# Performance work log

Hardware: AMD Instinct MI355X
Metric: run time of the kernel (lower is better)

Reference implementation:

```python
import jax, jax.numpy as jnp
import numpy as np

EXPR_MASK_RATIO = 0.4
POS_MASK_RATIO = 0.33
MIN_VISIBLE_GENES = 10


def setup_inputs() -> dict:
    key = jax.random.key(0)
    k1, k2 = jax.random.split(key)
    expression = jax.random.normal(k1, (16, 1024, 2000), dtype=jnp.float32)
    position = jax.random.normal(k2, (16, 1024, 3), dtype=jnp.float32)
    return {"expression": expression, "position": position}


def _expression_mask(expression, key):
    # strategy == 'random': rand matrix, kthvalue threshold, mask = rand >= threshold
    B, N, G = expression.shape
    num_masked = max(1, int(G * EXPR_MASK_RATIO))
    num_masked = min(num_masked, G - MIN_VISIBLE_GENES)
    rand = jax.random.uniform(key, (B, N, G), dtype=jnp.float32)
    # torch.kthvalue(rand, G - num_masked): (G - num_masked)-th smallest value,
    # i.e. index G - num_masked - 1 of the ascending sort (keepdim=True).
    kth = jnp.sort(rand, axis=-1)[..., G - num_masked - 1 : G - num_masked]  # (B,N,1)
    return rand >= kth  # bool (B,N,G); includes the threshold element, as in torch code


def _position_mask(position, key):
    # Vectorized form of the per-(b,n) loop:
    #   r < ratio*0.3      -> mask 2 of 3 dims (randperm(3)[:2] == complement of one uniform dim)
    #   ratio*0.3 <= r < ratio -> mask 1 uniform dim
    B, N, _ = position.shape
    kr, k1, k2 = jax.random.split(key, 3)
    r = jax.random.uniform(kr, (B, N), dtype=jnp.float32)
    two = r < POS_MASK_RATIO * 0.3
    one = (r < POS_MASK_RATIO) & (~two)
    dim1 = jax.random.randint(k1, (B, N), 0, 3)  # dim masked in the 1-dim branch
    excl = jax.random.randint(k2, (B, N), 0, 3)  # dim kept in the 2-dim branch
    eye = jnp.eye(3, dtype=bool)
    m1 = eye[dim1]        # (B,N,3) one-hot
    m2 = ~eye[excl]       # (B,N,3) two hot
    false3 = jnp.zeros((B, N, 3), dtype=bool)
    return jnp.where(two[..., None], m2, jnp.where(one[..., None], m1, false3))


def reference(expression, position):
    key = jax.random.key(42)
    ke, kp = jax.random.split(key)
    expr_mask = _expression_mask(expression, ke)   # (B,N,G) bool
    pos_mask = _position_mask(position, kp)        # (B,N,3) bool
    return expr_mask, pos_mask
```

## Files before the change

kernel.cpp:

```cpp
#include <hip/hip_runtime.h>
#include <stdint.h>

#define TF_ROUND(x0, x1, r)                    \
  {                                            \
    x0 += x1;                                  \
    x1 = (x1 << (r)) | (x1 >> (32 - (r)));     \
    x1 ^= x0;                                  \
  }

__host__ __device__ inline void threefry2x32(uint32_t k0, uint32_t k1,
                                             uint32_t x0, uint32_t x1,
                                             uint32_t& o0, uint32_t& o1) {
  const uint32_t ks2 = k0 ^ k1 ^ 0x1BD11BDAu;
  x0 += k0; x1 += k1;
  TF_ROUND(x0, x1, 13) TF_ROUND(x0, x1, 15) TF_ROUND(x0, x1, 26) TF_ROUND(x0, x1, 6)
  x0 += k1; x1 += ks2 + 1u;
  TF_ROUND(x0, x1, 17) TF_ROUND(x0, x1, 29) TF_ROUND(x0, x1, 16) TF_ROUND(x0, x1, 24)
  x0 += ks2; x1 += k0 + 2u;
  TF_ROUND(x0, x1, 13) TF_ROUND(x0, x1, 15) TF_ROUND(x0, x1, 26) TF_ROUND(x0, x1, 6)
  x0 += k0; x1 += k1 + 3u;
  TF_ROUND(x0, x1, 17) TF_ROUND(x0, x1, 29) TF_ROUND(x0, x1, 16) TF_ROUND(x0, x1, 24)
  x0 += k1; x1 += ks2 + 4u;
  TF_ROUND(x0, x1, 13) TF_ROUND(x0, x1, 15) TF_ROUND(x0, x1, 26) TF_ROUND(x0, x1, 6)
  x0 += ks2; x1 += k0 + 5u;
  o0 = x0; o1 = x1;
}

__device__ inline uint32_t random_bits32(uint32_t k0, uint32_t k1, uint32_t i) {
  uint32_t y0, y1;
  threefry2x32(k0, k1, 0u, i, y0, y1);
  return y0 ^ y1;
}

constexpr int B = 16;
constexpr int N = 1024;
constexpr int G = 2000;
constexpr int NUM_ROWS = B * N;
constexpr int RANK = G - 800 - 1;
constexpr long long EXPR_ELEMS = (long long)NUM_ROWS * G;

__global__ __launch_bounds__(256) void expr_mask_kernel(int32_t* __restrict__ out,
                                                        uint32_t ke0,
                                                        uint32_t ke1) {
  __shared__ uint32_t sm[G];
  __shared__ uint32_t hist[256];
  __shared__ uint32_t scan[256];
  __shared__ uint32_t cand[256];
  __shared__ uint32_t s_cnt;
  __shared__ uint32_t s_bucket;
  __shared__ uint32_t s_kk;
  __shared__ uint32_t s_thr;

  const int row = blockIdx.x;
  const int t = threadIdx.x;
  const long long rowbase = (long long)row * G;

  hist[t] = 0u;
  if (t == 0) s_cnt = 0u;
  __syncthreads();

  for (int g = t; g < G; g += 256) {
    uint32_t bits = random_bits32(ke0, ke1, (uint32_t)(rowbase + g));
    uint32_t m = bits >> 9;
    sm[g] = m;
    atomicAdd(&hist[m >> 15], 1u);
  }
  __syncthreads();

  uint32_t v = hist[t];
  scan[t] = v;
  __syncthreads();
  for (int off = 1; off < 256; off <<= 1) {
    uint32_t add = (t >= off) ? scan[t - off] : 0u;
    __syncthreads();
    scan[t] += add;
    __syncthreads();
  }
  uint32_t incl = scan[t];
  uint32_t excl = incl - v;
  if (excl <= (uint32_t)RANK && (uint32_t)RANK < incl) {
    s_bucket = (uint32_t)t;
    s_kk = (uint32_t)RANK - excl;
  }
  __syncthreads();

  const uint32_t bucket = s_bucket;
  for (int g = t; g < G; g += 256) {
    uint32_t m = sm[g];
    if ((m >> 15) == bucket) {
      uint32_t p = atomicAdd(&s_cnt, 1u);
      if (p < 256u) cand[p] = m;
    }
  }
  __syncthreads();

  const uint32_t c = (s_cnt < 256u) ? s_cnt : 256u;
  const uint32_t kk = s_kk;
  if ((uint32_t)t < c) {
    uint32_t mv = cand[t];
    uint32_t r = 0;
    for (uint32_t j = 0; j < c; ++j) {
      uint32_t mj = cand[j];
      r += (mj < mv) || (mj == mv && j < (uint32_t)t);
    }
    if (r == kk) s_thr = mv;
  }
  __syncthreads();

  const uint32_t thr = s_thr;
  for (int g = t; g < G; g += 256) {
    out[rowbase + g] = (sm[g] >= thr) ? 1 : 0;
  }
}

__global__ __launch_bounds__(256) void pos_mask_kernel(
    int32_t* __restrict__ out,
    uint32_t kr0, uint32_t kr1,
    uint32_t ah0, uint32_t ah1, uint32_t al0, uint32_t al1,
    uint32_t bh0, uint32_t bh1, uint32_t bl0, uint32_t bl1) {
  const int i = blockIdx.x * 256 + threadIdx.x;
  if (i >= NUM_ROWS) return;

  uint32_t rb = random_bits32(kr0, kr1, (uint32_t)i);
  union { uint32_t u; float f; } cvt;
  cvt.u = (rb >> 9) | 0x3F800000u;
  float r = cvt.f - 1.0f;

  const float THR2 = (float)(0.33 * 0.3);
  const float THR1 = (float)0.33;
  bool two = r < THR2;
  bool one = (r < THR1) && !two;

  uint32_t ah = random_bits32(ah0, ah1, (uint32_t)i);
  uint32_t al = random_bits32(al0, al1, (uint32_t)i);
  int dim1 = (int)(((ah % 3u) + (al % 3u)) % 3u);

  uint32_t bh = random_bits32(bh0, bh1, (uint32_t)i);
  uint32_t bl = random_bits32(bl0, bl1, (uint32_t)i);
  int excl = (int)(((bh % 3u) + (bl % 3u)) % 3u);

  int o[3];
#pragma unroll
  for (int d = 0; d < 3; ++d) {
    bool mval = two ? (d != excl) : (one ? (d == dim1) : false);
    o[d] = mval ? 1 : 0;
  }
  long long base = (long long)i * 3;
  out[base + 0] = o[0];
  out[base + 1] = o[1];
  out[base + 2] = o[2];
}

extern "C" void kernel_launch(void* const* d_in, const int* in_sizes, int n_in,
                              void* d_out, int out_size, void* d_ws, size_t ws_size,
                              hipStream_t stream) {
  (void)d_in; (void)in_sizes; (void)n_in; (void)d_ws; (void)ws_size; (void)out_size;

  uint32_t ke0, ke1, kp0, kp1;
  threefry2x32(0u, 42u, 0u, 0u, ke0, ke1);
  threefry2x32(0u, 42u, 0u, 1u, kp0, kp1);
  uint32_t kr0, kr1, ka0, ka1, kb0, kb1;
  threefry2x32(kp0, kp1, 0u, 0u, kr0, kr1);
  threefry2x32(kp0, kp1, 0u, 1u, ka0, ka1);
  threefry2x32(kp0, kp1, 0u, 2u, kb0, kb1);
  uint32_t ah0, ah1, al0, al1, bh0, bh1, bl0, bl1;
  threefry2x32(ka0, ka1, 0u, 0u, ah0, ah1);
  threefry2x32(ka0, ka1, 0u, 1u, al0, al1);
  threefry2x32(kb0, kb1, 0u, 0u, bh0, bh1);
  threefry2x32(kb0, kb1, 0u, 1u, bl0, bl1);

  int32_t* out_expr = (int32_t*)d_out;
  int32_t* out_pos = out_expr + EXPR_ELEMS;

  expr_mask_kernel<<<NUM_ROWS, 256, 0, stream>>>(out_expr, ke0, ke1);
  pos_mask_kernel<<<(NUM_ROWS + 255) / 256, 256, 0, stream>>>(
      out_pos, kr0, kr1, ah0, ah1, al0, al1, bh0, bh1, bl0, bl1);
}
```

Before: 267.3 us.

## Keep per-row random values in registers and store masks as int4

Each thread now owns 8 contiguous genes (250 active threads per row) and keeps their random mantissas in registers instead of a 2000-entry shared array. The per-row mask is written with two 16-byte int4 stores per thread instead of scalar strided stores. This removes the shared-memory staging, reduces LDS use and instructions, and widens global writes. Six of the 256 threads sit idle, and register pressure goes up slightly.

Result: faster. 246.0 us (-8.0%).

```diff
diff --git a/kernel.cpp b/kernel.cpp
--- a/kernel.cpp
+++ b/kernel.cpp
@@ -38,11 +38,12 @@
 constexpr int NUM_ROWS = B * N;
 constexpr int RANK = G - 800 - 1;
 constexpr long long EXPR_ELEMS = (long long)NUM_ROWS * G;
+constexpr int PER_THREAD = 8;
+constexpr int ACTIVE_T = G / PER_THREAD;
 
 __global__ __launch_bounds__(256) void expr_mask_kernel(int32_t* __restrict__ out,
                                                         uint32_t ke0,
                                                         uint32_t ke1) {
-  __shared__ uint32_t sm[G];
   __shared__ uint32_t hist[256];
   __shared__ uint32_t scan[256];
   __shared__ uint32_t cand[256];
@@ -51,19 +52,23 @@
   __shared__ uint32_t s_kk;
   __shared__ uint32_t s_thr;
 
-  const int row = blockIdx.x;
   const int t = threadIdx.x;
-  const long long rowbase = (long long)row * G;
+  const uint32_t rowstart = (uint32_t)blockIdx.x * (uint32_t)G;
+  const uint32_t base = rowstart + (uint32_t)t * (uint32_t)PER_THREAD;
+  const bool active = (t < ACTIVE_T);
 
   hist[t] = 0u;
   if (t == 0) s_cnt = 0u;
   __syncthreads();
 
-  for (int g = t; g < G; g += 256) {
-    uint32_t bits = random_bits32(ke0, ke1, (uint32_t)(rowbase + g));
-    uint32_t m = bits >> 9;
-    sm[g] = m;
-    atomicAdd(&hist[m >> 15], 1u);
+  uint32_t m[PER_THREAD];
+  if (active) {
+#pragma unroll
+    for (int j = 0; j < PER_THREAD; ++j) {
+      uint32_t bits = random_bits32(ke0, ke1, base + (uint32_t)j);
+      m[j] = bits >> 9;
+      atomicAdd(&hist[m[j] >> 15], 1u);
+    }
   }
   __syncthreads();
 
@@ -85,11 +90,13 @@
   __syncthreads();
 
   const uint32_t bucket = s_bucket;
-  for (int g = t; g < G; g += 256) {
-    uint32_t m = sm[g];
-    if ((m >> 15) == bucket) {
-      uint32_t p = atomicAdd(&s_cnt, 1u);
-      if (p < 256u) cand[p] = m;
+  if (active) {
+#pragma unroll
+    for (int j = 0; j < PER_THREAD; ++j) {
+      if ((m[j] >> 15) == bucket) {
+        uint32_t p = atomicAdd(&s_cnt, 1u);
+        if (p < 256u) cand[p] = m[j];
+      }
     }
   }
   __syncthreads();
@@ -108,8 +115,19 @@
   __syncthreads();
 
   const uint32_t thr = s_thr;
-  for (int g = t; g < G; g += 256) {
-    out[rowbase + g] = (sm[g] >= thr) ? 1 : 0;
+  if (active) {
+    int4 a, b;
+    a.x = (m[0] >= thr) ? 1 : 0;
+    a.y = (m[1] >= thr) ? 1 : 0;
+    a.z = (m[2] >= thr) ? 1 : 0;
+    a.w = (m[3] >= thr) ? 1 : 0;
+    b.x = (m[4] >= thr) ? 1 : 0;
+    b.y = (m[5] >= thr) ? 1 : 0;
+    b.z = (m[6] >= thr) ? 1 : 0;
+    b.w = (m[7] >= thr) ? 1 : 0;
+    int4* p = (int4*)(out + base);
+    p[0] = a;
+    p[1] = b;
   }
 }
 
@@ -145,10 +163,10 @@
     bool mval = two ? (d != excl) : (one ? (d == dim1) : false);
     o[d] = mval ? 1 : 0;
   }
-  long long base = (long long)i * 3;
-  out[base + 0] = o[0];
-  out[base + 1] = o[1];
-  out[base + 2] = o[2];
+  long long obase = (long long)i * 3;
+  out[obase + 0] = o[0];
+  out[obase + 1] = o[1];
+  out[obase + 2] = o[2];
 }
 
 extern "C" void kernel_launch(void* const* d_in, const int* in_sizes, int n_in,
```
